# Optimization experiments

Hardware: AMD Instinct MI355X
Metric: run time of the kernel (lower is better)

## Reference

```python
import jax, jax.numpy as jnp
import numpy as np

D_MODEL = 768
D_FF = 3072
N_HEADS = 12
HEAD_DIM = D_MODEL // N_HEADS
SUB_SCALE = 0.5
LN_EPS = 1e-5


def _layer_norm(x, g, b):
    mu = jnp.mean(x, axis=-1, keepdims=True)
    var = jnp.var(x, axis=-1, keepdims=True)
    return (x - mu) * jax.lax.rsqrt(var + LN_EPS) * g + b


def setup_inputs() -> dict:
    key = jax.random.key(0)
    ks = jax.random.split(key, 12)
    B, T = 1, 4096
    s = lambda fan_in: 1.0 / np.sqrt(fan_in)
    return {
        "x": jax.random.normal(ks[0], (B, T, D_MODEL), dtype=jnp.float32),
        "ln1_g": jnp.ones((D_MODEL,), jnp.float32),
        "ln1_b": jnp.zeros((D_MODEL,), jnp.float32),
        "ln2_g": jnp.ones((D_MODEL,), jnp.float32),
        "ln2_b": jnp.zeros((D_MODEL,), jnp.float32),
        "qkv_w": jax.random.normal(ks[1], (D_MODEL, 3 * D_MODEL), jnp.float32) * s(D_MODEL),
        "qkv_b": jnp.zeros((3 * D_MODEL,), jnp.float32),
        "out_w": jax.random.normal(ks[2], (D_MODEL, D_MODEL), jnp.float32) * s(D_MODEL),
        "out_b": jnp.zeros((D_MODEL,), jnp.float32),
        "fc1_w": jax.random.normal(ks[3], (D_MODEL, D_FF), jnp.float32) * s(D_MODEL),
        "fc1_b": jnp.zeros((D_FF,), jnp.float32),
        "fc2_w": jax.random.normal(ks[4], (D_FF, D_MODEL), jnp.float32) * s(D_FF),
        "fc2_b": jnp.zeros((D_MODEL,), jnp.float32),
    }


def reference(x, ln1_g, ln1_b, ln2_g, ln2_b, qkv_w, qkv_b, out_w, out_b,
              fc1_w, fc1_b, fc2_w, fc2_b):
    B, T, C = x.shape
    # --- attention sub-block ---
    h = _layer_norm(x, ln1_g, ln1_b) * SUB_SCALE
    qkv = h @ qkv_w + qkv_b                      # [B,T,3C]
    q, k, v = jnp.split(qkv, 3, axis=-1)
    split = lambda t: t.reshape(B, T, N_HEADS, HEAD_DIM).transpose(0, 2, 1, 3)
    q, k, v = split(q), split(k), split(v)       # [B,H,T,Hd]
    scores = jnp.einsum('bhqd,bhkd->bhqk', q, k) / jnp.sqrt(jnp.float32(HEAD_DIM))
    weights = jax.nn.softmax(scores, axis=-1)    # [B,H,T,T] (no mask, as in source)
    attn = jnp.einsum('bhqk,bhkd->bhqd', weights, v)
    attn = attn.transpose(0, 2, 1, 3).reshape(B, T, C)
    x = x + attn @ out_w + out_b
    # --- MLP sub-block ---
    h2 = _layer_norm(x, ln2_g, ln2_b) * SUB_SCALE
    h2 = jax.nn.gelu(h2 @ fc1_w + fc1_b, approximate=False)  # nn.GELU() = exact erf
    h2 = h2 @ fc2_w + fc2_b
    return x + h2
```

## Files before the change

kernel.cpp:

```cpp
#include <hip/hip_runtime.h>
#include <hip/hip_bf16.h>
#include <math.h>

#define TSEQ 4096
#define DMODEL 768
#define DFF 3072
#define NHEADS 12
#define HDIM 64

typedef __attribute__((ext_vector_type(8))) short short8;
typedef __attribute__((ext_vector_type(4))) float f32x4;
typedef unsigned short ushort;
typedef unsigned int uint;

typedef __attribute__((address_space(1))) ushort as1_ushort;
typedef __attribute__((address_space(3))) ushort as3_ushort;

__device__ __forceinline__ void gl_lds16(const ushort* g, const ushort* l) {
    __builtin_amdgcn_global_load_lds((as1_ushort*)(uintptr_t)g,
                                     (as3_ushort*)(uint)(uintptr_t)l, 16, 0, 0);
}

__device__ __forceinline__ ushort f2bf(float f) {
    union { float f; unsigned i; } c; c.f = f;
    unsigned x = c.i;
    unsigned r = x + 0x7FFFu + ((x >> 16) & 1u);
    return (ushort)(r >> 16);
}
__device__ __forceinline__ float asf(uint u) {
    union { unsigned i; float f; } c; c.i = u; return c.f;
}
__device__ __forceinline__ float gelu_fast(float v) {
    float y = v * (0.7978845608f + 0.03567740814f * v * v);
    float u = exp2f(y * -2.8853900817779268f);
    float r;
    asm("v_rcp_f32 %0, %1" : "=v"(r) : "v"(1.f + u));
    return v * r;
}

__global__ __launch_bounds__(256) void ln_half_kernel(
    const float* __restrict__ x, const float* __restrict__ g,
    const float* __restrict__ b, ushort* __restrict__ out)
{
    int row = blockIdx.x;
    const float* xr = x + (size_t)row * DMODEL;
    float v[3];
    float s = 0.f, s2 = 0.f;
    #pragma unroll
    for (int i = 0; i < 3; i++) {
        v[i] = xr[threadIdx.x + 256 * i];
        s += v[i]; s2 += v[i] * v[i];
    }
    #pragma unroll
    for (int m = 1; m < 64; m <<= 1) { s += __shfl_xor(s, m, 64); s2 += __shfl_xor(s2, m, 64); }
    __shared__ float ss[4], ss2[4];
    int wid = threadIdx.x >> 6;
    if ((threadIdx.x & 63) == 0) { ss[wid] = s; ss2[wid] = s2; }
    __syncthreads();
    s = ss[0] + ss[1] + ss[2] + ss[3];
    s2 = ss2[0] + ss2[1] + ss2[2] + ss2[3];
    float mu = s * (1.f / DMODEL);
    float var = s2 * (1.f / DMODEL) - mu * mu;
    float rs = rsqrtf(var + 1e-5f);
    #pragma unroll
    for (int i = 0; i < 3; i++) {
        int c = threadIdx.x + 256 * i;
        float h = (v[i] - mu) * rs * g[c] + b[c];
        out[(size_t)row * DMODEL + c] = f2bf(h * 0.5f);
    }
}

__global__ __launch_bounds__(256) void transpose_cast_kernel(
    const float* __restrict__ in, ushort* __restrict__ out, int K, int N)
{
    __shared__ float tile[32][33];
    int k0 = blockIdx.x * 32, n0 = blockIdx.y * 32;
    int c = threadIdx.x & 31, r0 = threadIdx.x >> 5;
    #pragma unroll
    for (int i = 0; i < 4; i++) {
        int r = r0 + i * 8;
        tile[r][c] = in[(size_t)(k0 + r) * N + n0 + c];
    }
    __syncthreads();
    #pragma unroll
    for (int i = 0; i < 4; i++) {
        int r = r0 + i * 8;
        out[(size_t)(n0 + r) * K + k0 + c] = f2bf(tile[c][r]);
    }
}

__global__ __launch_bounds__(256) void vtrans_kernel(
    const ushort* __restrict__ qkvb, ushort* __restrict__ vT)
{
    __shared__ ushort tile[64][72];
    int t0 = blockIdx.x * 64, d0 = blockIdx.y * 64;
    int tid = threadIdx.x;
    int r = tid >> 2, c = (tid & 3) * 16;
    const ushort* src = qkvb + (size_t)(t0 + r) * 2304 + 1536 + d0 + c;
    *(short8*)&tile[r][c]     = *(const short8*)src;
    *(short8*)&tile[r][c + 8] = *(const short8*)(src + 8);
    __syncthreads();
    int d = tid & 63, gq = tid >> 6;
    short8 w0, w1;
    #pragma unroll
    for (int i = 0; i < 8; i++) w0[i] = (short)tile[gq * 16 + i][d];
    #pragma unroll
    for (int i = 0; i < 8; i++) w1[i] = (short)tile[gq * 16 + 8 + i][d];
    ushort* dst = vT + (size_t)(d0 + d) * TSEQ + t0 + gq * 16;
    *(short8*)dst       = w0;
    *(short8*)(dst + 8) = w1;
}

template<int EPI>
__global__ __launch_bounds__(256) void gemm_kernel(
    const ushort* __restrict__ A, const ushort* __restrict__ Bt,
    const float* __restrict__ bias, const float* __restrict__ res,
    void* __restrict__ out, int M, int N, int K)
{
    __shared__ ushort As[2][128 * 32];
    __shared__ ushort Bs[2][128 * 32];
    int bm = blockIdx.x * 128, bn = blockIdx.y * 128;
    int tid = threadIdx.x;
    int wid = tid >> 6, lane = tid & 63;
    int wm = (wid >> 1) * 64, wn = (wid & 1) * 64;
    int lg = lane >> 4, lr = lane & 15;
    int srow = lane >> 2, scol = (lane & 3) * 8;
    f32x4 acc[4][4] = {};

    const ushort* ga0 = A  + (size_t)(bm + wid * 16 + srow) * K + scol;
    const ushort* ga1 = A  + (size_t)(bm + 64 + wid * 16 + srow) * K + scol;
    const ushort* gb0 = Bt + (size_t)(bn + wid * 16 + srow) * K + scol;
    const ushort* gb1 = Bt + (size_t)(bn + 64 + wid * 16 + srow) * K + scol;

    gl_lds16(ga0, &As[0][wid * 512]);
    gl_lds16(ga1, &As[0][2048 + wid * 512]);
    gl_lds16(gb0, &Bs[0][wid * 512]);
    gl_lds16(gb1, &Bs[0][2048 + wid * 512]);

    int nt = K >> 5;
    for (int t = 0; t < nt; t++) {
        int cur = t & 1;
        __syncthreads();
        if (t + 1 < nt) {
            int k0 = (t + 1) << 5;
            int nb = cur ^ 1;
            gl_lds16(ga0 + k0, &As[nb][wid * 512]);
            gl_lds16(ga1 + k0, &As[nb][2048 + wid * 512]);
            gl_lds16(gb0 + k0, &Bs[nb][wid * 512]);
            gl_lds16(gb1 + k0, &Bs[nb][2048 + wid * 512]);
        }
        short8 a[4], b[4];
        #pragma unroll
        for (int mi = 0; mi < 4; mi++) a[mi] = *(const short8*)&As[cur][(wm + mi * 16 + lr) * 32 + lg * 8];
        #pragma unroll
        for (int ni = 0; ni < 4; ni++) b[ni] = *(const short8*)&Bs[cur][(wn + ni * 16 + lr) * 32 + lg * 8];
        #pragma unroll
        for (int mi = 0; mi < 4; mi++)
            #pragma unroll
            for (int ni = 0; ni < 4; ni++)
                acc[mi][ni] = __builtin_amdgcn_mfma_f32_16x16x32_bf16(a[mi], b[ni], acc[mi][ni], 0, 0, 0);
    }

    #pragma unroll
    for (int mi = 0; mi < 4; mi++) {
        #pragma unroll
        for (int ni = 0; ni < 4; ni++) {
            int col = bn + wn + ni * 16 + lr;
            float bv = bias[col];
            #pragma unroll
            for (int r = 0; r < 4; r++) {
                int row = bm + wm + mi * 16 + lg * 4 + r;
                float v = acc[mi][ni][r] + bv;
                size_t idx = (size_t)row * N + col;
                if (EPI == 0) {
                    ((ushort*)out)[idx] = f2bf(v);
                } else if (EPI == 1) {
                    ((ushort*)out)[idx] = f2bf(gelu_fast(v));
                } else {
                    ((float*)out)[idx] = v + res[idx];
                }
            }
        }
    }
}

template<int EPI>
__global__ __launch_bounds__(256) void gemm_n64_kernel(
    const ushort* __restrict__ A, const ushort* __restrict__ Bt,
    const float* __restrict__ bias, const float* __restrict__ res,
    void* __restrict__ out, int M, int N, int K)
{
    __shared__ ushort As[2][128 * 32];
    __shared__ ushort Bs[2][64 * 32];
    int bm = blockIdx.x * 128, bn = blockIdx.y * 64;
    int tid = threadIdx.x;
    int wid = tid >> 6, lane = tid & 63;
    int wm = (wid >> 1) * 64, wn = (wid & 1) * 32;
    int lg = lane >> 4, lr = lane & 15;
    int srow = lane >> 2, scol = (lane & 3) * 8;
    f32x4 acc[4][2] = {};

    const ushort* ga0 = A  + (size_t)(bm + wid * 16 + srow) * K + scol;
    const ushort* ga1 = A  + (size_t)(bm + 64 + wid * 16 + srow) * K + scol;
    const ushort* gb0 = Bt + (size_t)(bn + wid * 16 + srow) * K + scol;

    gl_lds16(ga0, &As[0][wid * 512]);
    gl_lds16(ga1, &As[0][2048 + wid * 512]);
    gl_lds16(gb0, &Bs[0][wid * 512]);

    int nt = K >> 5;
    for (int t = 0; t < nt; t++) {
        int cur = t & 1;
        __syncthreads();
        if (t + 1 < nt) {
            int k0 = (t + 1) << 5;
            int nb = cur ^ 1;
            gl_lds16(ga0 + k0, &As[nb][wid * 512]);
            gl_lds16(ga1 + k0, &As[nb][2048 + wid * 512]);
            gl_lds16(gb0 + k0, &Bs[nb][wid * 512]);
        }
        short8 a[4], b[2];
        #pragma unroll
        for (int mi = 0; mi < 4; mi++) a[mi] = *(const short8*)&As[cur][(wm + mi * 16 + lr) * 32 + lg * 8];
        #pragma unroll
        for (int ni = 0; ni < 2; ni++) b[ni] = *(const short8*)&Bs[cur][(wn + ni * 16 + lr) * 32 + lg * 8];
        #pragma unroll
        for (int mi = 0; mi < 4; mi++)
            #pragma unroll
            for (int ni = 0; ni < 2; ni++)
                acc[mi][ni] = __builtin_amdgcn_mfma_f32_16x16x32_bf16(a[mi], b[ni], acc[mi][ni], 0, 0, 0);
    }

    #pragma unroll
    for (int mi = 0; mi < 4; mi++) {
        #pragma unroll
        for (int ni = 0; ni < 2; ni++) {
            int col = bn + wn + ni * 16 + lr;
            float bv = bias[col];
            #pragma unroll
            for (int r = 0; r < 4; r++) {
                int row = bm + wm + mi * 16 + lg * 4 + r;
                float v = acc[mi][ni][r] + bv;
                size_t idx = (size_t)row * N + col;
                if (EPI == 0) {
                    ((ushort*)out)[idx] = f2bf(v);
                } else if (EPI == 1) {
                    ((ushort*)out)[idx] = f2bf(gelu_fast(v));
                } else {
                    ((float*)out)[idx] = v + res[idx];
                }
            }
        }
    }
}

__global__ __launch_bounds__(512) void attn_kernel(
    const ushort* __restrict__ qkv, const ushort* __restrict__ vT,
    ushort* __restrict__ Opart, float* __restrict__ ml)
{
    int h = blockIdx.y;
    int qblk = blockIdx.x;
    int split = blockIdx.z;
    __shared__ ushort Ks[2][64 * 64];
    __shared__ ushort Vt[2][64 * 64];
    __shared__ ushort Ps[256 * 72];
    int tid = threadIdx.x, wid = tid >> 6, lane = tid & 63;
    int lg = lane >> 4, lr = lane & 15;
    const float C1 = 0.18033688011112042f;
    const float KC = 12.0f * C1;

    {
        int row = tid >> 1, cc = (tid & 1) * 32;
        const ushort* src = qkv + (size_t)(qblk * 256 + row) * 2304 + h * HDIM + cc;
        *(short8*)&Ps[row * 72 + cc]      = *(const short8*)src;
        *(short8*)&Ps[row * 72 + cc + 8]  = *(const short8*)(src + 8);
        *(short8*)&Ps[row * 72 + cc + 16] = *(const short8*)(src + 16);
        *(short8*)&Ps[row * 72 + cc + 24] = *(const short8*)(src + 24);
    }
    int prow0 = (wid * 32 + lr) * 72;
    int prow1 = prow0 + 16 * 72;
    short8 qa0 = *(const short8*)&Ps[prow0 + lg * 8];
    short8 qa1 = *(const short8*)&Ps[prow0 + 32 + lg * 8];
    short8 qb0 = *(const short8*)&Ps[prow1 + lg * 8];
    short8 qb1 = *(const short8*)&Ps[prow1 + 32 + lg * 8];

    short8 vone;
    #pragma unroll
    for (int i = 0; i < 8; i++) vone[i] = (short)0x3F80;

    int krow = tid >> 3;
    int kunit = (tid & 7) ^ (krow & 7);
    const ushort* kg = qkv + (size_t)(split * 1024 + krow) * 2304 + DMODEL + h * HDIM + kunit * 8;
    const ushort* vgp = vT + (size_t)(h * HDIM + krow) * TSEQ + split * 1024 + kunit * 8;

    gl_lds16(kg, &Ks[0][tid * 8]);
    gl_lds16(vgp, &Vt[0][tid * 8]);
    kg += 64 * 2304;
    vgp += 64;

    f32x4 o0[4] = {}, o1[4] = {};
    f32x4 s0sum = {}, s1sum = {};
    const int NT = 16;
    int x7 = lr & 7;

    for (int kt = 0; kt < NT; kt++) {
        int cur = kt & 1, nb = cur ^ 1;
        __syncthreads();
        if (kt + 1 < NT) {
            gl_lds16(kg, &Ks[nb][tid * 8]);
            gl_lds16(vgp, &Vt[nb][tid * 8]);
            kg += 64 * 2304;
            vgp += 64;
        }

        f32x4 st0[4] = {}, st1[4] = {};
        #pragma unroll
        for (int ki = 0; ki < 4; ki++) {
            const ushort* kr = &Ks[cur][(ki * 16 + lr) * 64];
            short8 k0 = *(const short8*)&kr[(lg ^ x7) * 8];
            short8 k1 = *(const short8*)&kr[((4 + lg) ^ x7) * 8];
            st0[ki] = __builtin_amdgcn_mfma_f32_16x16x32_bf16(k0, qa0, st0[ki], 0, 0, 0);
            st0[ki] = __builtin_amdgcn_mfma_f32_16x16x32_bf16(k1, qa1, st0[ki], 0, 0, 0);
            st1[ki] = __builtin_amdgcn_mfma_f32_16x16x32_bf16(k0, qb0, st1[ki], 0, 0, 0);
            st1[ki] = __builtin_amdgcn_mfma_f32_16x16x32_bf16(k1, qb1, st1[ki], 0, 0, 0);
        }

        #pragma unroll
        for (int ki = 0; ki < 4; ki++) {
            #pragma unroll
            for (int r = 0; r < 4; r++) st0[ki][r] = exp2f(st0[ki][r] * C1 - KC);
            uint d0, d1;
            asm("v_cvt_pk_bf16_f32 %0, %1, %2" : "=v"(d0) : "v"(st0[ki][0]), "v"(st0[ki][1]));
            asm("v_cvt_pk_bf16_f32 %0, %1, %2" : "=v"(d1) : "v"(st0[ki][2]), "v"(st0[ki][3]));
            *(uint*)&Ps[prow0 + ki * 16 + lg * 4]     = d0;
            *(uint*)&Ps[prow0 + ki * 16 + lg * 4 + 2] = d1;
        }
        #pragma unroll
        for (int ki = 0; ki < 4; ki++) {
            #pragma unroll
            for (int r = 0; r < 4; r++) st1[ki][r] = exp2f(st1[ki][r] * C1 - KC);
            uint d0, d1;
            asm("v_cvt_pk_bf16_f32 %0, %1, %2" : "=v"(d0) : "v"(st1[ki][0]), "v"(st1[ki][1]));
            asm("v_cvt_pk_bf16_f32 %0, %1, %2" : "=v"(d1) : "v"(st1[ki][2]), "v"(st1[ki][3]));
            *(uint*)&Ps[prow1 + ki * 16 + lg * 4]     = d0;
            *(uint*)&Ps[prow1 + ki * 16 + lg * 4 + 2] = d1;
        }

        short8 pa00 = *(const short8*)&Ps[prow0 + lg * 8];
        short8 pa01 = *(const short8*)&Ps[prow0 + 32 + lg * 8];
        short8 pa10 = *(const short8*)&Ps[prow1 + lg * 8];
        short8 pa11 = *(const short8*)&Ps[prow1 + 32 + lg * 8];

        s0sum = __builtin_amdgcn_mfma_f32_16x16x32_bf16(pa00, vone, s0sum, 0, 0, 0);
        s0sum = __builtin_amdgcn_mfma_f32_16x16x32_bf16(pa01, vone, s0sum, 0, 0, 0);
        s1sum = __builtin_amdgcn_mfma_f32_16x16x32_bf16(pa10, vone, s1sum, 0, 0, 0);
        s1sum = __builtin_amdgcn_mfma_f32_16x16x32_bf16(pa11, vone, s1sum, 0, 0, 0);

        #pragma unroll
        for (int ni = 0; ni < 4; ni++) {
            const ushort* vr = &Vt[cur][(ni * 16 + lr) * 64];
            short8 b0 = *(const short8*)&vr[(lg ^ x7) * 8];
            short8 b1 = *(const short8*)&vr[((4 + lg) ^ x7) * 8];
            o0[ni] = __builtin_amdgcn_mfma_f32_16x16x32_bf16(pa00, b0, o0[ni], 0, 0, 0);
            o0[ni] = __builtin_amdgcn_mfma_f32_16x16x32_bf16(pa01, b1, o0[ni], 0, 0, 0);
            o1[ni] = __builtin_amdgcn_mfma_f32_16x16x32_bf16(pa10, b0, o1[ni], 0, 0, 0);
            o1[ni] = __builtin_amdgcn_mfma_f32_16x16x32_bf16(pa11, b1, o1[ni], 0, 0, 0);
        }
    }

    if (lr == 0) {
        #pragma unroll
        for (int r = 0; r < 4; r++) {
            int q0 = qblk * 256 + wid * 32 + lg * 4 + r;
            ml[((size_t)split * NHEADS + h) * TSEQ + q0]      = s0sum[r];
            ml[((size_t)split * NHEADS + h) * TSEQ + q0 + 16] = s1sum[r];
        }
    }
    #pragma unroll
    for (int ni = 0; ni < 4; ni++)
        #pragma unroll
        for (int r = 0; r < 4; r++) {
            int q0 = qblk * 256 + wid * 32 + lg * 4 + r;
            int dcol = ni * 16 + lr;
            Opart[((size_t)split * TSEQ + q0) * DMODEL + h * HDIM + dcol]      = f2bf(o0[ni][r]);
            Opart[((size_t)split * TSEQ + q0 + 16) * DMODEL + h * HDIM + dcol] = f2bf(o1[ni][r]);
        }
}

__global__ __launch_bounds__(256) void attn_combine_kernel(
    const ushort* __restrict__ Opart, const float* __restrict__ ml,
    ushort* __restrict__ attnb)
{
    int gid = blockIdx.x * 256 + threadIdx.x;
    int q = gid / 192;
    int c = (gid - q * 192) * 4;
    int hh = c >> 6;
    float denom = 0.f;
    float a0 = 0.f, a1 = 0.f, a2 = 0.f, a3 = 0.f;
    #pragma unroll
    for (int s = 0; s < 4; s++) {
        denom += ml[((size_t)s * NHEADS + hh) * TSEQ + q];
        uint2 ov = *(const uint2*)&Opart[((size_t)s * TSEQ + q) * DMODEL + c];
        a0 += asf(ov.x << 16);
        a1 += asf(ov.x & 0xFFFF0000u);
        a2 += asf(ov.y << 16);
        a3 += asf(ov.y & 0xFFFF0000u);
    }
    float rd = 1.f / denom;
    uint2 stv;
    stv.x = (uint)f2bf(a0 * rd) | ((uint)f2bf(a1 * rd) << 16);
    stv.y = (uint)f2bf(a2 * rd) | ((uint)f2bf(a3 * rd) << 16);
    *(uint2*)&attnb[(size_t)q * DMODEL + c] = stv;
}

extern "C" void kernel_launch(void* const* d_in, const int* in_sizes, int n_in,
                              void* d_out, int out_size, void* d_ws, size_t ws_size,
                              hipStream_t stream)
{
    const float* x      = (const float*)d_in[0];
    const float* ln1_g  = (const float*)d_in[1];
    const float* ln1_b  = (const float*)d_in[2];
    const float* ln2_g  = (const float*)d_in[3];
    const float* ln2_b  = (const float*)d_in[4];
    const float* qkv_w  = (const float*)d_in[5];
    const float* qkv_b  = (const float*)d_in[6];
    const float* out_w  = (const float*)d_in[7];
    const float* out_b  = (const float*)d_in[8];
    const float* fc1_w  = (const float*)d_in[9];
    const float* fc1_b  = (const float*)d_in[10];
    const float* fc2_w  = (const float*)d_in[11];
    const float* fc2_b  = (const float*)d_in[12];
    (void)in_sizes; (void)n_in; (void)out_size; (void)ws_size;

    char* p = (char*)d_ws;
    ushort* qkvb  = (ushort*)p;                 p += (size_t)TSEQ * DFF * 2;
    ushort* hb    = (ushort*)p;                 p += (size_t)TSEQ * DMODEL * 2;
    ushort* attnb = (ushort*)p;                 p += (size_t)TSEQ * DMODEL * 2;
    float*  x2    = (float*)p;                  p += (size_t)TSEQ * DMODEL * 4;
    ushort* qkv_wT = (ushort*)p;                p += (size_t)(3 * DMODEL) * DMODEL * 2;
    ushort* out_wT = (ushort*)p;                p += (size_t)DMODEL * DMODEL * 2;
    ushort* fc1_wT = (ushort*)p;                p += (size_t)DFF * DMODEL * 2;
    ushort* fc2_wT = (ushort*)p;                p += (size_t)DMODEL * DFF * 2;
    ushort* Opart  = (ushort*)p;                p += (size_t)4 * TSEQ * DMODEL * 2;
    float*  mlbuf  = (float*)p;                 p += (size_t)4 * NHEADS * TSEQ * 4;
    ushort* vTb    = (ushort*)p;                p += (size_t)DMODEL * TSEQ * 2;
    ushort* gb = qkvb;

    transpose_cast_kernel<<<dim3(DMODEL / 32, 3 * DMODEL / 32), 256, 0, stream>>>(qkv_w, qkv_wT, DMODEL, 3 * DMODEL);
    transpose_cast_kernel<<<dim3(DMODEL / 32, DMODEL / 32), 256, 0, stream>>>(out_w, out_wT, DMODEL, DMODEL);
    transpose_cast_kernel<<<dim3(DMODEL / 32, DFF / 32), 256, 0, stream>>>(fc1_w, fc1_wT, DMODEL, DFF);
    transpose_cast_kernel<<<dim3(DFF / 32, DMODEL / 32), 256, 0, stream>>>(fc2_w, fc2_wT, DFF, DMODEL);

    ln_half_kernel<<<TSEQ, 256, 0, stream>>>(x, ln1_g, ln1_b, hb);
    gemm_kernel<0><<<dim3(TSEQ / 128, 3 * DMODEL / 128), 256, 0, stream>>>(
        hb, qkv_wT, qkv_b, nullptr, qkvb, TSEQ, 3 * DMODEL, DMODEL);
    vtrans_kernel<<<dim3(TSEQ / 64, DMODEL / 64), 256, 0, stream>>>(qkvb, vTb);
    attn_kernel<<<dim3(TSEQ / 256, NHEADS, 4), 512, 0, stream>>>(qkvb, vTb, Opart, mlbuf);
    attn_combine_kernel<<<(TSEQ * DMODEL / 4) / 256, 256, 0, stream>>>(Opart, mlbuf, attnb);
    gemm_n64_kernel<2><<<dim3(TSEQ / 128, DMODEL / 64), 256, 0, stream>>>(
        attnb, out_wT, out_b, x, x2, TSEQ, DMODEL, DMODEL);
    ln_half_kernel<<<TSEQ, 256, 0, stream>>>(x2, ln2_g, ln2_b, hb);
    gemm_kernel<1><<<dim3(TSEQ / 128, DFF / 128), 256, 0, stream>>>(
        hb, fc1_wT, fc1_b, nullptr, gb, TSEQ, DFF, DMODEL);
    gemm_n64_kernel<2><<<dim3(TSEQ / 128, DMODEL / 64), 256, 0, stream>>>(
        gb, fc2_wT, fc2_b, x2, (float*)d_out, TSEQ, DMODEL, DFF);
}
```

Baseline: 219.6 us.

## Shrink attention LDS footprint and split P staging into halves with priority hints

Merges the K, V and P shared buffers into one array. Q is now staged through the K region with an XOR swizzle, so the P scratch only needs half-width rows (40 instead of 72 ushorts). P is written and reread in two 32-column halves, each consumed by its own MFMA group. The launch bound now asks for 6 waves per SIMD and s_setprio hints are wrapped around the MFMA sections. The goal is higher occupancy and better overlap of exp work with matrix work, at the risk of register spills under the tighter launch bound.

```diff
diff --git a/kernel.cpp b/kernel.cpp
--- a/kernel.cpp
+++ b/kernel.cpp
@@ -254,35 +254,40 @@
     }
 }
 
-__global__ __launch_bounds__(512) void attn_kernel(
+__global__ __launch_bounds__(512, 6) void attn_kernel(
     const ushort* __restrict__ qkv, const ushort* __restrict__ vT,
     ushort* __restrict__ Opart, float* __restrict__ ml)
 {
     int h = blockIdx.y;
     int qblk = blockIdx.x;
     int split = blockIdx.z;
-    __shared__ ushort Ks[2][64 * 64];
-    __shared__ ushort Vt[2][64 * 64];
-    __shared__ ushort Ps[256 * 72];
+    __shared__ ushort smem[16384 + 256 * 40];
+    ushort* Ps = smem + 16384;
     int tid = threadIdx.x, wid = tid >> 6, lane = tid & 63;
     int lg = lane >> 4, lr = lane & 15;
     const float C1 = 0.18033688011112042f;
     const float KC = 12.0f * C1;
+    int x7 = lr & 15 & 7;
+    x7 = lr & 7;
 
     {
-        int row = tid >> 1, cc = (tid & 1) * 32;
-        const ushort* src = qkv + (size_t)(qblk * 256 + row) * 2304 + h * HDIM + cc;
-        *(short8*)&Ps[row * 72 + cc]      = *(const short8*)src;
-        *(short8*)&Ps[row * 72 + cc + 8]  = *(const short8*)(src + 8);
-        *(short8*)&Ps[row * 72 + cc + 16] = *(const short8*)(src + 16);
-        *(short8*)&Ps[row * 72 + cc + 24] = *(const short8*)(src + 24);
-    }
-    int prow0 = (wid * 32 + lr) * 72;
-    int prow1 = prow0 + 16 * 72;
-    short8 qa0 = *(const short8*)&Ps[prow0 + lg * 8];
-    short8 qa1 = *(const short8*)&Ps[prow0 + 32 + lg * 8];
-    short8 qb0 = *(const short8*)&Ps[prow1 + lg * 8];
-    short8 qb1 = *(const short8*)&Ps[prow1 + 32 + lg * 8];
+        int row = tid >> 1;
+        int u0 = (tid & 1) * 4;
+        int r7 = row & 7;
+        const ushort* src = qkv + (size_t)(qblk * 256 + row) * 2304 + h * HDIM;
+        #pragma unroll
+        for (int i = 0; i < 4; i++) {
+            int u = u0 + i;
+            *(short8*)&smem[row * 64 + u * 8] = *(const short8*)(src + (size_t)((u ^ r7) * 8));
+        }
+    }
+    int q0row = (wid * 32 + lr) * 64;
+    int q1row = q0row + 16 * 64;
+    short8 qa0 = *(const short8*)&smem[q0row + (lg ^ x7) * 8];
+    short8 qa1 = *(const short8*)&smem[q0row + ((4 + lg) ^ x7) * 8];
+    short8 qb0 = *(const short8*)&smem[q1row + (lg ^ x7) * 8];
+    short8 qb1 = *(const short8*)&smem[q1row + ((4 + lg) ^ x7) * 8];
+    __syncthreads();
 
     short8 vone;
     #pragma unroll
@@ -293,30 +298,34 @@
     const ushort* kg = qkv + (size_t)(split * 1024 + krow) * 2304 + DMODEL + h * HDIM + kunit * 8;
     const ushort* vgp = vT + (size_t)(h * HDIM + krow) * TSEQ + split * 1024 + kunit * 8;
 
-    gl_lds16(kg, &Ks[0][tid * 8]);
-    gl_lds16(vgp, &Vt[0][tid * 8]);
+    gl_lds16(kg, &smem[tid * 8]);
+    gl_lds16(vgp, &smem[8192 + tid * 8]);
     kg += 64 * 2304;
     vgp += 64;
 
     f32x4 o0[4] = {}, o1[4] = {};
     f32x4 s0sum = {}, s1sum = {};
     const int NT = 16;
-    int x7 = lr & 7;
+    int prow0 = (wid * 32 + lr) * 40;
+    int prow1 = prow0 + 16 * 40;
 
     for (int kt = 0; kt < NT; kt++) {
         int cur = kt & 1, nb = cur ^ 1;
         __syncthreads();
         if (kt + 1 < NT) {
-            gl_lds16(kg, &Ks[nb][tid * 8]);
-            gl_lds16(vgp, &Vt[nb][tid * 8]);
+            gl_lds16(kg, &smem[nb * 4096 + tid * 8]);
+            gl_lds16(vgp, &smem[8192 + nb * 4096 + tid * 8]);
             kg += 64 * 2304;
             vgp += 64;
         }
+        const ushort* kb = &smem[cur * 4096];
+        const ushort* vb = &smem[8192 + cur * 4096];
 
         f32x4 st0[4] = {}, st1[4] = {};
+        __builtin_amdgcn_s_setprio(1);
         #pragma unroll
         for (int ki = 0; ki < 4; ki++) {
-            const ushort* kr = &Ks[cur][(ki * 16 + lr) * 64];
+            const ushort* kr = &kb[(ki * 16 + lr) * 64];
             short8 k0 = *(const short8*)&kr[(lg ^ x7) * 8];
             short8 k1 = *(const short8*)&kr[((4 + lg) ^ x7) * 8];
             st0[ki] = __builtin_amdgcn_mfma_f32_16x16x32_bf16(k0, qa0, st0[ki], 0, 0, 0);
@@ -324,47 +333,59 @@
             st1[ki] = __builtin_amdgcn_mfma_f32_16x16x32_bf16(k0, qb0, st1[ki], 0, 0, 0);
             st1[ki] = __builtin_amdgcn_mfma_f32_16x16x32_bf16(k1, qb1, st1[ki], 0, 0, 0);
         }
-
+        __builtin_amdgcn_s_setprio(0);
+
+        uint2 c0[4], c1[4];
         #pragma unroll
         for (int ki = 0; ki < 4; ki++) {
             #pragma unroll
             for (int r = 0; r < 4; r++) st0[ki][r] = exp2f(st0[ki][r] * C1 - KC);
-            uint d0, d1;
-            asm("v_cvt_pk_bf16_f32 %0, %1, %2" : "=v"(d0) : "v"(st0[ki][0]), "v"(st0[ki][1]));
-            asm("v_cvt_pk_bf16_f32 %0, %1, %2" : "=v"(d1) : "v"(st0[ki][2]), "v"(st0[ki][3]));
-            *(uint*)&Ps[prow0 + ki * 16 + lg * 4]     = d0;
-            *(uint*)&Ps[prow0 + ki * 16 + lg * 4 + 2] = d1;
+            asm("v_cvt_pk_bf16_f32 %0, %1, %2" : "=v"(c0[ki].x) : "v"(st0[ki][0]), "v"(st0[ki][1]));
+            asm("v_cvt_pk_bf16_f32 %0, %1, %2" : "=v"(c0[ki].y) : "v"(st0[ki][2]), "v"(st0[ki][3]));
         }
         #pragma unroll
         for (int ki = 0; ki < 4; ki++) {
             #pragma unroll
             for (int r = 0; r < 4; r++) st1[ki][r] = exp2f(st1[ki][r] * C1 - KC);
-            uint d0, d1;
-            asm("v_cvt_pk_bf16_f32 %0, %1, %2" : "=v"(d0) : "v"(st1[ki][0]), "v"(st1[ki][1]));
-            asm("v_cvt_pk_bf16_f32 %0, %1, %2" : "=v"(d1) : "v"(st1[ki][2]), "v"(st1[ki][3]));
-            *(uint*)&Ps[prow1 + ki * 16 + lg * 4]     = d0;
-            *(uint*)&Ps[prow1 + ki * 16 + lg * 4 + 2] = d1;
-        }
-
-        short8 pa00 = *(const short8*)&Ps[prow0 + lg * 8];
-        short8 pa01 = *(const short8*)&Ps[prow0 + 32 + lg * 8];
-        short8 pa10 = *(const short8*)&Ps[prow1 + lg * 8];
-        short8 pa11 = *(const short8*)&Ps[prow1 + 32 + lg * 8];
-
-        s0sum = __builtin_amdgcn_mfma_f32_16x16x32_bf16(pa00, vone, s0sum, 0, 0, 0);
-        s0sum = __builtin_amdgcn_mfma_f32_16x16x32_bf16(pa01, vone, s0sum, 0, 0, 0);
-        s1sum = __builtin_amdgcn_mfma_f32_16x16x32_bf16(pa10, vone, s1sum, 0, 0, 0);
-        s1sum = __builtin_amdgcn_mfma_f32_16x16x32_bf16(pa11, vone, s1sum, 0, 0, 0);
-
-        #pragma unroll
-        for (int ni = 0; ni < 4; ni++) {
-            const ushort* vr = &Vt[cur][(ni * 16 + lr) * 64];
-            short8 b0 = *(const short8*)&vr[(lg ^ x7) * 8];
-            short8 b1 = *(const short8*)&vr[((4 + lg) ^ x7) * 8];
-            o0[ni] = __builtin_amdgcn_mfma_f32_16x16x32_bf16(pa00, b0, o0[ni], 0, 0, 0);
-            o0[ni] = __builtin_amdgcn_mfma_f32_16x16x32_bf16(pa01, b1, o0[ni], 0, 0, 0);
-            o1[ni] = __builtin_amdgcn_mfma_f32_16x16x32_bf16(pa10, b0, o1[ni], 0, 0, 0);
-            o1[ni] = __builtin_amdgcn_mfma_f32_16x16x32_bf16(pa11, b1, o1[ni], 0, 0, 0);
+            asm("v_cvt_pk_bf16_f32 %0, %1, %2" : "=v"(c1[ki].x) : "v"(st1[ki][0]), "v"(st1[ki][1]));
+            asm("v_cvt_pk_bf16_f32 %0, %1, %2" : "=v"(c1[ki].y) : "v"(st1[ki][2]), "v"(st1[ki][3]));
+        }
+
+        *(uint2*)&Ps[prow0 + lg * 4]      = c0[0];
+        *(uint2*)&Ps[prow0 + 16 + lg * 4] = c0[1];
+        *(uint2*)&Ps[prow1 + lg * 4]      = c1[0];
+        *(uint2*)&Ps[prow1 + 16 + lg * 4] = c1[1];
+        {
+            short8 pa00 = *(const short8*)&Ps[prow0 + lg * 8];
+            short8 pa10 = *(const short8*)&Ps[prow1 + lg * 8];
+            __builtin_amdgcn_s_setprio(1);
+            s0sum = __builtin_amdgcn_mfma_f32_16x16x32_bf16(pa00, vone, s0sum, 0, 0, 0);
+            s1sum = __builtin_amdgcn_mfma_f32_16x16x32_bf16(pa10, vone, s1sum, 0, 0, 0);
+            #pragma unroll
+            for (int ni = 0; ni < 4; ni++) {
+                short8 b0 = *(const short8*)&vb[(ni * 16 + lr) * 64 + (lg ^ x7) * 8];
+                o0[ni] = __builtin_amdgcn_mfma_f32_16x16x32_bf16(pa00, b0, o0[ni], 0, 0, 0);
+                o1[ni] = __builtin_amdgcn_mfma_f32_16x16x32_bf16(pa10, b0, o1[ni], 0, 0, 0);
+            }
+            __builtin_amdgcn_s_setprio(0);
+        }
+        *(uint2*)&Ps[prow0 + lg * 4]      = c0[2];
+        *(uint2*)&Ps[prow0 + 16 + lg * 4] = c0[3];
+        *(uint2*)&Ps[prow1 + lg * 4]      = c1[2];
+        *(uint2*)&Ps[prow1 + 16 + lg * 4] = c1[3];
+        {
+            short8 pa01 = *(const short8*)&Ps[prow0 + lg * 8];
+            short8 pa11 = *(const short8*)&Ps[prow1 + lg * 8];
+            __builtin_amdgcn_s_setprio(1);
+            s0sum = __builtin_amdgcn_mfma_f32_16x16x32_bf16(pa01, vone, s0sum, 0, 0, 0);
+            s1sum = __builtin_amdgcn_mfma_f32_16x16x32_bf16(pa11, vone, s1sum, 0, 0, 0);
+            #pragma unroll
+            for (int ni = 0; ni < 4; ni++) {
+                short8 b1 = *(const short8*)&vb[(ni * 16 + lr) * 64 + ((4 + lg) ^ x7) * 8];
+                o0[ni] = __builtin_amdgcn_mfma_f32_16x16x32_bf16(pa01, b1, o0[ni], 0, 0, 0);
+                o1[ni] = __builtin_amdgcn_mfma_f32_16x16x32_bf16(pa11, b1, o1[ni], 0, 0, 0);
+            }
+            __builtin_amdgcn_s_setprio(0);
         }
     }
 
```

After: 462.7 us. 2.11x slower.
